# Optimization experiments

Measured on AMD Instinct MI355X. Metric: run time of the kernel, lower is better.

The kernel has to match this reference:

```python
import jax, jax.numpy as jnp
import numpy as np

HEADS = 4
HID = 128            # hidden_channels
D = HID // HEADS     # per-head dim = 32
IN = 128
OUT = 64
NEG = 0.2            # PyG HANConv default negative_slope
N_AUTHOR = 100000
N_PAPER = 200000
E = 1000000


def setup_inputs() -> dict:
    key = jax.random.key(0)
    ks = jax.random.split(key, 24)
    g = lambda i, shape, s=1.0: jax.random.normal(ks[i], shape, jnp.float32) * s
    ri = lambda i, hi: jax.random.randint(ks[i], (E,), 0, hi, dtype=jnp.int64)
    sp = float(1.0 / np.sqrt(IN))
    sh = float(1.0 / np.sqrt(HID))
    return dict(
        x_author=g(0, (N_AUTHOR, IN)),
        x_paper=g(1, (N_PAPER, IN)),
        writes_src=ri(13, N_AUTHOR), writes_dst=ri(14, N_PAPER),
        writtenby_src=ri(15, N_PAPER), writtenby_dst=ri(16, N_AUTHOR),
        cites_src=ri(17, N_PAPER), cites_dst=ri(18, N_PAPER),
        W_proj_author=g(2, (IN, HID), sp), b_proj_author=jnp.zeros((HID,), jnp.float32),
        W_proj_paper=g(3, (IN, HID), sp), b_proj_paper=jnp.zeros((HID,), jnp.float32),
        att_src_writes=g(4, (HEADS, D), sh), att_dst_writes=g(5, (HEADS, D), sh),
        att_src_writtenby=g(6, (HEADS, D), sh), att_dst_writtenby=g(7, (HEADS, D), sh),
        att_src_cites=g(8, (HEADS, D), sh), att_dst_cites=g(9, (HEADS, D), sh),
        W_k=g(10, (HID, HID), sh), b_k=jnp.zeros((HID,), jnp.float32),
        q=g(11, (HID,), sh),
        W_lin=g(12, (HID, OUT), sh), b_lin=jnp.zeros((OUT,), jnp.float32),
    )


def _edge_conv(x_src, x_dst, att_s, att_d, src, dst, n_dst):
    # x_src: [Ns,H,D], x_dst: [Nd,H,D]; gather-attend-(segment softmax)-scatter
    a_s = jnp.einsum('nhd,hd->nh', x_src, att_s)[src]   # [E,H]
    a_d = jnp.einsum('nhd,hd->nh', x_dst, att_d)[dst]   # [E,H]
    alpha = jax.nn.leaky_relu(a_s + a_d, NEG)
    m = jax.ops.segment_max(alpha, dst, num_segments=n_dst)      # [Nd,H]
    ex = jnp.exp(alpha - m[dst])
    den = jax.ops.segment_sum(ex, dst, num_segments=n_dst)
    alpha = ex / (den[dst] + 1e-16)
    msg = (x_src[src] * alpha[:, :, None]).reshape(-1, HID)      # [E,HID]
    out = jax.ops.segment_sum(msg, dst, num_segments=n_dst)      # [Nd,HID]
    return jax.nn.relu(out)


def _group(outs, q, W_k, b_k):
    # semantic-level attention over edge types (PyG HANConv `group`)
    out = jnp.stack(outs)                                         # [T,N,HID]
    score = (q * jnp.tanh(out @ W_k + b_k).mean(axis=1)).sum(-1)  # [T]
    attn = jax.nn.softmax(score)
    return jnp.einsum('t,tnc->nc', attn, out)


def reference(x_author, x_paper, writes_src, writes_dst, writtenby_src,
              writtenby_dst, cites_src, cites_dst, W_proj_author,
              b_proj_author, W_proj_paper, b_proj_paper, att_src_writes,
              att_dst_writes, att_src_writtenby, att_dst_writtenby,
              att_src_cites, att_dst_cites, W_k, b_k, q, W_lin, b_lin):
    h_a = (x_author @ W_proj_author + b_proj_author).reshape(-1, HEADS, D)
    h_p = (x_paper @ W_proj_paper + b_proj_paper).reshape(-1, HEADS, D)
    o_writes = _edge_conv(h_a, h_p, att_src_writes, att_dst_writes,
                          writes_src, writes_dst, N_PAPER)
    o_wb = _edge_conv(h_p, h_a, att_src_writtenby, att_dst_writtenby,
                      writtenby_src, writtenby_dst, N_AUTHOR)
    o_cites = _edge_conv(h_p, h_p, att_src_cites, att_dst_cites,
                         cites_src, cites_dst, N_PAPER)
    out_author = _group([o_wb], q, W_k, b_k)
    out_paper = _group([o_writes, o_cites], q, W_k, b_k)
    # final per-node-type shared Linear (HANModel.lin)
    return (out_author @ W_lin + b_lin, out_paper @ W_lin + b_lin)
```

## Files before the change

kernel.cpp:

```cpp
#include <hip/hip_runtime.h>
#include <hip/hip_bf16.h>


#define HEADS 4
#define DH 32
#define HID 128
#define IN_F 128
#define OUT_F 64
#define NEG 0.2f

typedef unsigned short u16;
typedef unsigned int u32;
typedef __attribute__((ext_vector_type(8))) short short8;
typedef __attribute__((ext_vector_type(4))) float f32x4;

__device__ __forceinline__ float us2f(u16 u){ return __uint_as_float(((u32)u) << 16); }
__device__ __forceinline__ u16 f2us(float f){
  u32 u = __float_as_uint(f);
  u += 0x7fffu + ((u >> 16) & 1u);
  return (u16)(u >> 16);
}
__device__ __forceinline__ float fin(float v){ return (fabsf(v) < 1e30f) ? v : 0.f; }
__device__ __forceinline__ u16 san16(u16 r){ return (((r >> 7) & 0xff) == 0xff) ? (u16)0 : r; }
__device__ __forceinline__ float ftanh(float x){
  float t = __expf(fminf(fmaxf(2.f * x, -30.f), 30.f));
  return __fdividef(t - 1.f, t + 1.f);
}
__device__ __forceinline__ float ldf(const void* p, size_t i, int wide){
  float v = wide ? ((const float*)p)[i] : us2f(((const u16*)p)[i]);
  return fin(v);
}
__device__ __forceinline__ u16 ld16(const void* p, size_t i, int wide){
  if (wide) return f2us(fin(((const float*)p)[i]));
  return san16(((const u16*)p)[i]);
}
__device__ __forceinline__ int ld_idx(const int* __restrict__ p, int e, int sh, int n){
  int v = p[(size_t)e << sh];
  return v < 0 ? 0 : (v >= n ? n - 1 : v);
}

__global__ void detect_float_width(const u16* __restrict__ x, int n, int* __restrict__ flag)
{
  __shared__ int cnt;
  if (threadIdx.x == 0) cnt = 0;
  __syncthreads();
  int local = 0;
  for (int i = threadIdx.x; i < n; i += blockDim.x) {
    int e = (x[i] >> 7) & 0xff;
    if (e == 0 || (e >= 100 && e <= 150)) local++;
  }
  atomicAdd(&cnt, local);
  __syncthreads();
  if (threadIdx.x == 0) *flag = (cnt < (n * 9) / 10) ? 1 : 0;
}
__global__ void detect_idx_width(const int* __restrict__ s, int n, int* __restrict__ flag)
{
  __shared__ int any;
  if (threadIdx.x == 0) any = 0;
  __syncthreads();
  for (int i = threadIdx.x; i < n; i += blockDim.x)
    if (s[2 * i + 1] != 0) atomicOr(&any, 1);
  __syncthreads();
  if (threadIdx.x == 0) *flag = any ? 0 : 1;
}

template<int NC>
__device__ __forceinline__ void stage_B1(const void* W1, int wide, u16* Bt)
{
  for (int i = threadIdx.x; i < 128 * NC; i += 256) {
    int k = i / NC, c = i - k * NC;
    u16 v = ld16(W1, (size_t)k * NC + c, wide);
    u32 boff = ((u32)c << 8) + (((u32)(k << 1)) ^ (((u32)(c & 7)) << 4));
    *(u16*)((char*)Bt + boff) = v;
  }
}

__device__ __forceinline__ short8 ldsB(const u16* Bt, int t, int lane, int kk)
{
  const int c = (t << 4) + (lane & 15);
  const u32 boff = ((u32)c << 8) +
      (((u32)(((lane >> 4) << 4) + (kk << 6))) ^ (((u32)(c & 7)) << 4));
  return *(const short8*)((const char*)Bt + boff);
}

__device__ __forceinline__ short8 ldA_x(const void* x, size_t rb, int kg, int kk, int wide)
{
  short8 v;
  const size_t base = rb + (size_t)(kg * 8 + kk * 32);
  if (wide) {
    const float* p = (const float*)x + base;
    const float4 f0 = *(const float4*)p;
    const float4 f1 = *(const float4*)(p + 4);
    v[0] = (short)f2us(fin(f0.x)); v[1] = (short)f2us(fin(f0.y));
    v[2] = (short)f2us(fin(f0.z)); v[3] = (short)f2us(fin(f0.w));
    v[4] = (short)f2us(fin(f1.x)); v[5] = (short)f2us(fin(f1.y));
    v[6] = (short)f2us(fin(f1.z)); v[7] = (short)f2us(fin(f1.w));
  } else {
    const short8 raw = *(const short8*)((const u16*)x + base);
#pragma unroll
    for (int j = 0; j < 8; ++j) v[j] = (short)san16((u16)raw[j]);
  }
  return v;
}

__device__ __forceinline__ short8 ldA_o(const u16* o, size_t rb, int kg, int kk)
{
  return *(const short8*)(o + rb + (size_t)(kg * 8 + kk * 32));
}

__global__ __launch_bounds__(256, 2) void proj_mfma(
    const void* __restrict__ x, const void* __restrict__ W,
    const void* __restrict__ b, u16* __restrict__ h, int N,
    const int* __restrict__ flag_f)
{
  const int wide = *flag_f;
  __shared__ u16 Bt[128 * 128];
  stage_B1<HID>(W, wide, Bt);
  __syncthreads();
  const int w = threadIdx.x >> 6, lane = threadIdx.x & 63;
  const int r16 = lane & 15, kg = lane >> 4;
  float bv[8];
#pragma unroll
  for (int t = 0; t < 8; ++t) bv[t] = ldf(b, (t << 4) + r16, wide);
  const int nstrips = (N + 63) >> 6;
  for (int sidx = blockIdx.x; sidx < nstrips; sidx += gridDim.x) {
    const int rowbase = (sidx << 6) + (w << 4);
    int arow = rowbase + r16;
    if (arow >= N) arow = N - 1;
    const size_t rb = (size_t)arow * IN_F;
    f32x4 acc[8];
#pragma unroll
    for (int t = 0; t < 8; ++t) acc[t] = (f32x4){0.f, 0.f, 0.f, 0.f};
#pragma unroll
    for (int kk = 0; kk < 4; ++kk) {
      const short8 a = ldA_x(x, rb, kg, kk, wide);
#pragma unroll
      for (int t = 0; t < 8; ++t)
        acc[t] = __builtin_amdgcn_mfma_f32_16x16x32_bf16(a, ldsB(Bt, t, lane, kk), acc[t], 0, 0, 0);
    }
#pragma unroll
    for (int t = 0; t < 8; ++t) {
      const int col = (t << 4) + r16;
#pragma unroll
      for (int j = 0; j < 4; ++j) {
        const int row = rowbase + (kg << 2) + j;
        if (row < N) h[(size_t)row * HID + col] = f2us(acc[t][j] + bv[t]);
      }
    }
  }
}

__global__ __launch_bounds__(256, 2) void colsum_mfma(
    const u16* __restrict__ o, int rows, const void* __restrict__ Wk,
    const void* __restrict__ bk, float* __restrict__ S,
    const int* __restrict__ flag_f)
{
  const int wide = *flag_f;
  __shared__ u16 Bt[128 * 128];
  __shared__ float sred[4][HID];
  stage_B1<HID>(Wk, wide, Bt);
  __syncthreads();
  const int w = threadIdx.x >> 6, lane = threadIdx.x & 63;
  const int r16 = lane & 15, kg = lane >> 4;
  float bkv[8];
#pragma unroll
  for (int t = 0; t < 8; ++t) bkv[t] = ldf(bk, (t << 4) + r16, wide);
  float scs[8] = {0.f, 0.f, 0.f, 0.f, 0.f, 0.f, 0.f, 0.f};
  const int nstrips = (rows + 63) >> 6;
  for (int sidx = blockIdx.x; sidx < nstrips; sidx += gridDim.x) {
    const int rowbase = (sidx << 6) + (w << 4);
    int arow = rowbase + r16;
    if (arow >= rows) arow = rows - 1;
    const size_t rb = (size_t)arow * HID;
    f32x4 acc[8];
#pragma unroll
    for (int t = 0; t < 8; ++t) acc[t] = (f32x4){0.f, 0.f, 0.f, 0.f};
#pragma unroll
    for (int kk = 0; kk < 4; ++kk) {
      const short8 a = ldA_o(o, rb, kg, kk);
#pragma unroll
      for (int t = 0; t < 8; ++t)
        acc[t] = __builtin_amdgcn_mfma_f32_16x16x32_bf16(a, ldsB(Bt, t, lane, kk), acc[t], 0, 0, 0);
    }
#pragma unroll
    for (int t = 0; t < 8; ++t) {
#pragma unroll
      for (int j = 0; j < 4; ++j) {
        const int row = rowbase + (kg << 2) + j;
        if (row < rows) scs[t] += ftanh(acc[t][j] + bkv[t]);
      }
    }
  }
#pragma unroll
  for (int t = 0; t < 8; ++t) {
    float v = scs[t];
    v += __shfl_xor(v, 16);
    v += __shfl_xor(v, 32);
    if (kg == 0) sred[w][(t << 4) + r16] = v;
  }
  __syncthreads();
  if (threadIdx.x < HID) {
    float v = sred[0][threadIdx.x] + sred[1][threadIdx.x] +
              sred[2][threadIdx.x] + sred[3][threadIdx.x];
    atomicAdd(&S[threadIdx.x], v);
  }
}

__global__ __launch_bounds__(256, 2) void linW_mfma(
    const u16* __restrict__ o, int rows, const void* __restrict__ Wlin,
    u16* __restrict__ P, const int* __restrict__ flag_f)
{
  const int wide = *flag_f;
  __shared__ u16 Bt[64 * 128];
  stage_B1<OUT_F>(Wlin, wide, Bt);
  __syncthreads();
  const int w = threadIdx.x >> 6, lane = threadIdx.x & 63;
  const int r16 = lane & 15, kg = lane >> 4;
  const int nstrips = (rows + 63) >> 6;
  for (int sidx = blockIdx.x; sidx < nstrips; sidx += gridDim.x) {
    const int rowbase = (sidx << 6) + (w << 4);
    int arow = rowbase + r16;
    if (arow >= rows) arow = rows - 1;
    const size_t rb = (size_t)arow * HID;
    f32x4 acc[4];
#pragma unroll
    for (int t = 0; t < 4; ++t) acc[t] = (f32x4){0.f, 0.f, 0.f, 0.f};
#pragma unroll
    for (int kk = 0; kk < 4; ++kk) {
      const short8 a = ldA_o(o, rb, kg, kk);
#pragma unroll
      for (int t = 0; t < 4; ++t)
        acc[t] = __builtin_amdgcn_mfma_f32_16x16x32_bf16(a, ldsB(Bt, t, lane, kk), acc[t], 0, 0, 0);
    }
#pragma unroll
    for (int t = 0; t < 4; ++t) {
      const int col = (t << 4) + r16;
#pragma unroll
      for (int j = 0; j < 4; ++j) {
        const int row = rowbase + (kg << 2) + j;
        if (row < rows) P[(size_t)row * OUT_F + col] = f2us(acc[t][j]);
      }
    }
  }
}

__global__ __launch_bounds__(256, 2) void author_mfma(
    const u16* __restrict__ o, int rows, int node0,
    const void* __restrict__ Wlin, const void* __restrict__ blin,
    void* __restrict__ out, const int* __restrict__ flag_f)
{
  const int wide = *flag_f;
  __shared__ u16 Bt[64 * 128];
  stage_B1<OUT_F>(Wlin, wide, Bt);
  __syncthreads();
  const int w = threadIdx.x >> 6, lane = threadIdx.x & 63;
  const int r16 = lane & 15, kg = lane >> 4;
  float bv[4];
#pragma unroll
  for (int t = 0; t < 4; ++t) bv[t] = ldf(blin, (t << 4) + r16, wide);
  const int nstrips = (rows + 63) >> 6;
  for (int sidx = blockIdx.x; sidx < nstrips; sidx += gridDim.x) {
    const int rowbase = (sidx << 6) + (w << 4);
    int arow = rowbase + r16;
    if (arow >= rows) arow = rows - 1;
    const size_t rb = (size_t)arow * HID;
    f32x4 acc[4];
#pragma unroll
    for (int t = 0; t < 4; ++t) acc[t] = (f32x4){0.f, 0.f, 0.f, 0.f};
#pragma unroll
    for (int kk = 0; kk < 4; ++kk) {
      const short8 a = ldA_o(o, rb, kg, kk);
#pragma unroll
      for (int t = 0; t < 4; ++t)
        acc[t] = __builtin_amdgcn_mfma_f32_16x16x32_bf16(a, ldsB(Bt, t, lane, kk), acc[t], 0, 0, 0);
    }
#pragma unroll
    for (int t = 0; t < 4; ++t) {
      const int col = (t << 4) + r16;
#pragma unroll
      for (int j = 0; j < 4; ++j) {
        const int row = rowbase + (kg << 2) + j;
        if (row < rows) {
          const float val = acc[t][j] + bv[t];
          const size_t oi = (size_t)(node0 + row) * OUT_F + col;
          if (wide) ((float*)out)[oi] = val;
          else      ((u16*)out)[oi] = f2us(val);
        }
      }
    }
  }
}

__global__ __launch_bounds__(256) void compute_a2(
    const u16* __restrict__ h, const void* __restrict__ att1,
    const void* __restrict__ att2, float* __restrict__ a1,
    float* __restrict__ a2, int N, const int* __restrict__ flag_f)
{
  const int wide = *flag_f;
  __shared__ float s1[HID], s2[HID];
  if (threadIdx.x < HID) {
    s1[threadIdx.x] = ldf(att1, threadIdx.x, wide);
    s2[threadIdx.x] = ldf(att2, threadIdx.x, wide);
  }
  __syncthreads();
  int t = blockIdx.x * 256 + threadIdx.x;
  if (t >= N * HEADS) return;
  int n = t >> 2, hh = t & 3;
  const u16* p = h + (size_t)n * HID + hh * DH;
  float acc1 = 0.f, acc2 = 0.f;
#pragma unroll
  for (int d = 0; d < DH; ++d) {
    float f = us2f(p[d]);
    acc1 += f * s1[hh * DH + d];
    acc2 += f * s2[hh * DH + d];
  }
  a1[t] = fin(acc1);
  a2[t] = fin(acc2);
}

__global__ __launch_bounds__(256) void compute_a4(
    const u16* __restrict__ h,
    const void* __restrict__ att1, const void* __restrict__ att2,
    const void* __restrict__ att3, const void* __restrict__ att4,
    float* __restrict__ a1, float* __restrict__ a2,
    float* __restrict__ a3, float* __restrict__ a4,
    int N, const int* __restrict__ flag_f)
{
  const int wide = *flag_f;
  __shared__ float s1[HID], s2[HID], s3[HID], s4[HID];
  if (threadIdx.x < HID) {
    s1[threadIdx.x] = ldf(att1, threadIdx.x, wide);
    s2[threadIdx.x] = ldf(att2, threadIdx.x, wide);
    s3[threadIdx.x] = ldf(att3, threadIdx.x, wide);
    s4[threadIdx.x] = ldf(att4, threadIdx.x, wide);
  }
  __syncthreads();
  int t = blockIdx.x * 256 + threadIdx.x;
  if (t >= N * HEADS) return;
  int n = t >> 2, hh = t & 3;
  const u16* p = h + (size_t)n * HID + hh * DH;
  float acc1 = 0.f, acc2 = 0.f, acc3 = 0.f, acc4 = 0.f;
#pragma unroll
  for (int d = 0; d < DH; ++d) {
    float f = us2f(p[d]);
    int c = hh * DH + d;
    acc1 += f * s1[c];
    acc2 += f * s2[c];
    acc3 += f * s3[c];
    acc4 += f * s4[c];
  }
  a1[t] = fin(acc1);
  a2[t] = fin(acc2);
  a3[t] = fin(acc3);
  a4[t] = fin(acc4);
}

__global__ __launch_bounds__(256) void hist3_part(
    const int* __restrict__ d0, int E0, int N0, int* __restrict__ g0,
    const int* __restrict__ d1, int E1, int N1, int* __restrict__ g1,
    const int* __restrict__ d2, int E2, int N2, int* __restrict__ g2,
    const int* __restrict__ flag_i)
{
  const int part = blockIdx.x & 7;
  const int grp  = blockIdx.x >> 3;
  const int ngrp = gridDim.x >> 3;
  const int sh = *flag_i;
  for (int e = grp * 256 + threadIdx.x; e < E0; e += ngrp * 256) {
    int d = ld_idx(d0, e, sh, N0);
    if ((d * 8) / N0 == part) atomicAdd(&g0[d], 1);
  }
  for (int e = grp * 256 + threadIdx.x; e < E1; e += ngrp * 256) {
    int d = ld_idx(d1, e, sh, N1);
    if ((d * 8) / N1 == part) atomicAdd(&g1[d], 1);
  }
  for (int e = grp * 256 + threadIdx.x; e < E2; e += ngrp * 256) {
    int d = ld_idx(d2, e, sh, N2);
    if ((d * 8) / N2 == part) atomicAdd(&g2[d], 1);
  }
}

__global__ __launch_bounds__(256) void scan1_kernel(
    const int* __restrict__ deg, int Nd, int* __restrict__ rowptr,
    int* __restrict__ blksum)
{
  __shared__ int ssum[256];
  int base = blockIdx.x * 1024;
  int t = threadIdx.x;
  int idx0 = base + t * 4;
  int v[4];
#pragma unroll
  for (int j = 0; j < 4; ++j) v[j] = (idx0 + j < Nd) ? deg[idx0 + j] : 0;
  int tsum = v[0] + v[1] + v[2] + v[3];
  ssum[t] = tsum;
  __syncthreads();
  for (int ofs = 1; ofs < 256; ofs <<= 1) {
    int x = (t >= ofs) ? ssum[t - ofs] : 0;
    __syncthreads();
    ssum[t] += x;
    __syncthreads();
  }
  if (t == 255) blksum[blockIdx.x] = ssum[255];
  int run = ssum[t] - tsum;
#pragma unroll
  for (int j = 0; j < 4; ++j) {
    if (idx0 + j < Nd) rowptr[idx0 + j] = run;
    run += v[j];
  }
}

__global__ void scan2x3_kernel(int* __restrict__ b0, int n0,
                               int* __restrict__ b1, int n1,
                               int* __restrict__ b2, int n2)
{
  if (blockIdx.x == 0) {
    if (threadIdx.x == 0) { int r = 0; for (int i = 0; i < n0; ++i) { int t = b0[i]; b0[i] = r; r += t; } }
    if (threadIdx.x == 1) { int r = 0; for (int i = 0; i < n1; ++i) { int t = b1[i]; b1[i] = r; r += t; } }
    if (threadIdx.x == 2) { int r = 0; for (int i = 0; i < n2; ++i) { int t = b2[i]; b2[i] = r; r += t; } }
  }
}

__global__ __launch_bounds__(256) void scan3_kernel(
    int* __restrict__ rowptr, int* __restrict__ cursor,
    const int* __restrict__ blksum, int Nd, int E)
{
  int i = blockIdx.x * 256 + threadIdx.x;
  if (i < Nd) {
    int v = rowptr[i] + blksum[i >> 10];
    rowptr[i] = v;
    cursor[i] = v;
  }
  if (i == 0) rowptr[Nd] = E;
}

__global__ __launch_bounds__(256) void reorder3_part(
    const int* __restrict__ s0, const int* __restrict__ d0, int E0, int Ns0, int N0,
    int* __restrict__ c0, int* __restrict__ o0,
    const int* __restrict__ s1, const int* __restrict__ d1, int E1, int Ns1, int N1,
    int* __restrict__ c1, int* __restrict__ o1,
    const int* __restrict__ s2, const int* __restrict__ d2, int E2, int Ns2, int N2,
    int* __restrict__ c2, int* __restrict__ o2,
    const int* __restrict__ flag_i)
{
  const int part = blockIdx.x & 7;
  const int grp  = blockIdx.x >> 3;
  const int ngrp = gridDim.x >> 3;
  const int sh = *flag_i;
  for (int e = grp * 256 + threadIdx.x; e < E0; e += ngrp * 256) {
    int d = ld_idx(d0, e, sh, N0);
    if ((d * 8) / N0 == part) {
      int s = ld_idx(s0, e, sh, Ns0);
      o0[atomicAdd(&c0[d], 1)] = s;
    }
  }
  for (int e = grp * 256 + threadIdx.x; e < E1; e += ngrp * 256) {
    int d = ld_idx(d1, e, sh, N1);
    if ((d * 8) / N1 == part) {
      int s = ld_idx(s1, e, sh, Ns1);
      o1[atomicAdd(&c1[d], 1)] = s;
    }
  }
  for (int e = grp * 256 + threadIdx.x; e < E2; e += ngrp * 256) {
    int d = ld_idx(d2, e, sh, N2);
    if ((d * 8) / N2 == part) {
      int s = ld_idx(s2, e, sh, Ns2);
      o2[atomicAdd(&c2[d], 1)] = s;
    }
  }
}

__global__ __launch_bounds__(256) void gather_conv(
    const int* __restrict__ rowptr, const int* __restrict__ csr_src,
    const float* __restrict__ a_s, const float* __restrict__ a_d,
    const u16* __restrict__ h_src, u16* __restrict__ o,
    int lo, int rows)
{
  int wid = (blockIdx.x * 256 + threadIdx.x) >> 6;
  if (wid >= rows) return;
  int n = lo + wid;
  int lane = threadIdx.x & 63;
  int hh = lane >> 4;
  int start = rowptr[n], end = rowptr[n + 1];
  float ad = a_d[(size_t)n * HEADS + hh];
  float m = -1e30f, den = 0.f, n0 = 0.f, n1 = 0.f;
  int e = start;
  for (; e + 4 <= end; e += 4) {
    int s0 = csr_src[e],     s1 = csr_src[e + 1];
    int s2 = csr_src[e + 2], s3 = csr_src[e + 3];
    float x0 = a_s[(size_t)s0 * HEADS + hh] + ad;
    float x1 = a_s[(size_t)s1 * HEADS + hh] + ad;
    float x2 = a_s[(size_t)s2 * HEADS + hh] + ad;
    float x3 = a_s[(size_t)s3 * HEADS + hh] + ad;
    ushort2 h0 = *(const ushort2*)(h_src + (size_t)s0 * HID + 2 * lane);
    ushort2 h1 = *(const ushort2*)(h_src + (size_t)s1 * HID + 2 * lane);
    ushort2 h2 = *(const ushort2*)(h_src + (size_t)s2 * HID + 2 * lane);
    ushort2 h3 = *(const ushort2*)(h_src + (size_t)s3 * HID + 2 * lane);
    x0 = (x0 > 0.f) ? x0 : NEG * x0;
    x1 = (x1 > 0.f) ? x1 : NEG * x1;
    x2 = (x2 > 0.f) ? x2 : NEG * x2;
    x3 = (x3 > 0.f) ? x3 : NEG * x3;
    float mloc = fmaxf(fmaxf(x0, x1), fmaxf(x2, x3));
    float mn = fmaxf(m, mloc);
    float sc = __expf(m - mn);
    float e0 = __expf(x0 - mn), e1 = __expf(x1 - mn);
    float e2 = __expf(x2 - mn), e3 = __expf(x3 - mn);
    den = den * sc + ((e0 + e1) + (e2 + e3));
    n0  = n0 * sc + (e0 * us2f(h0.x) + e1 * us2f(h1.x))
                  + (e2 * us2f(h2.x) + e3 * us2f(h3.x));
    n1  = n1 * sc + (e0 * us2f(h0.y) + e1 * us2f(h1.y))
                  + (e2 * us2f(h2.y) + e3 * us2f(h3.y));
    m = mn;
  }
  for (; e < end; ++e) {
    int s = csr_src[e];
    float x = a_s[(size_t)s * HEADS + hh] + ad;
    ushort2 hv = *(const ushort2*)(h_src + (size_t)s * HID + 2 * lane);
    x = (x > 0.f) ? x : NEG * x;
    float mn = fmaxf(m, x);
    float sc = __expf(m - mn);
    float ex = __expf(x - mn);
    den = den * sc + ex;
    n0  = n0 * sc + ex * us2f(hv.x);
    n1  = n1 * sc + ex * us2f(hv.y);
    m = mn;
  }
  float inv = 1.f / (den + 1e-16f);
  ushort2 st;
  st.x = f2us(fmaxf(n0 * inv, 0.f));
  st.y = f2us(fmaxf(n1 * inv, 0.f));
  *(ushort2*)(o + (size_t)wid * HID + 2 * lane) = st;
}

__global__ void score_softmax(const float* __restrict__ S, const void* __restrict__ q,
                              float* __restrict__ attn, float invN,
                              const int* __restrict__ flag_f)
{
  if (threadIdx.x == 0 && blockIdx.x == 0) {
    const int wide = *flag_f;
    float s0 = 0.f, s1 = 0.f;
    for (int c = 0; c < HID; ++c) {
      float qc = ldf(q, c, wide);
      s0 += qc * S[c] * invN;
      s1 += qc * S[HID + c] * invN;
    }
    float m = fmaxf(s0, s1);
    float e0 = __expf(s0 - m), e1 = __expf(s1 - m);
    attn[0] = e0 / (e0 + e1);
    attn[1] = e1 / (e0 + e1);
  }
}

__global__ __launch_bounds__(256) void combine_paper(
    const u16* __restrict__ Pw, const u16* __restrict__ Pc,
    const float* __restrict__ attn, const void* __restrict__ blin,
    void* __restrict__ out, size_t elem_off, int N,
    const int* __restrict__ flag_f)
{
  int t = blockIdx.x * 256 + threadIdx.x;
  if (t >= N * 16) return;
  const int wide = *flag_f;
  int n = t >> 4, cq = t & 15;
  const float a0 = attn[0], a1 = attn[1];
  size_t i = (size_t)n * OUT_F + cq * 4;
  ushort4 w4 = *(const ushort4*)&Pw[i];
  ushort4 c4 = *(const ushort4*)&Pc[i];
  float v[4];
  v[0] = a0 * us2f(w4.x) + a1 * us2f(c4.x) + ldf(blin, cq * 4 + 0, wide);
  v[1] = a0 * us2f(w4.y) + a1 * us2f(c4.y) + ldf(blin, cq * 4 + 1, wide);
  v[2] = a0 * us2f(w4.z) + a1 * us2f(c4.z) + ldf(blin, cq * 4 + 2, wide);
  v[3] = a0 * us2f(w4.w) + a1 * us2f(c4.w) + ldf(blin, cq * 4 + 3, wide);
  size_t oi = elem_off + i;
  if (wide) {
    float4 ov = {v[0], v[1], v[2], v[3]};
    *(float4*)&((float*)out)[oi] = ov;
  } else {
    ushort4 ov;
    ov.x = f2us(v[0]); ov.y = f2us(v[1]); ov.z = f2us(v[2]); ov.w = f2us(v[3]);
    *(ushort4*)&((u16*)out)[oi] = ov;
  }
}

extern "C" void kernel_launch(void* const* d_in, const int* in_sizes, int n_in,
                              void* d_out, int out_size, void* d_ws, size_t ws_size,
                              hipStream_t stream)
{
  const int NA = in_sizes[0] / IN_F;
  const int NP = in_sizes[1] / IN_F;
  const int E_w = in_sizes[2], E_wb = in_sizes[4], E_c = in_sizes[6];

  const void* x_a   = d_in[0];
  const void* x_p   = d_in[1];
  const int* w_src  = (const int*)d_in[2];
  const int* w_dst  = (const int*)d_in[3];
  const int* wb_src = (const int*)d_in[4];
  const int* wb_dst = (const int*)d_in[5];
  const int* c_src  = (const int*)d_in[6];
  const int* c_dst  = (const int*)d_in[7];
  const void* W_pa  = d_in[8];
  const void* b_pa  = d_in[9];
  const void* W_pp  = d_in[10];
  const void* b_pp  = d_in[11];
  const void* at_s_w  = d_in[12];
  const void* at_d_w  = d_in[13];
  const void* at_s_wb = d_in[14];
  const void* at_d_wb = d_in[15];
  const void* at_s_c  = d_in[16];
  const void* at_d_c  = d_in[17];
  const void* W_k   = d_in[18];
  const void* b_k   = d_in[19];
  const void* q     = d_in[20];
  const void* W_lin = d_in[21];
  const void* b_lin = d_in[22];

  char* ws = (char*)d_ws;
  size_t off = 0;
  auto alloc = [&](size_t bytes) -> void* {
    void* p = ws + off;
    off += (bytes + 255) & ~(size_t)255;
    return p;
  };
  int*   flag_f = (int*)alloc(4);
  int*   flag_i = (int*)alloc(4);
  float* attn   = (float*)alloc(8 * 4);
  float* S      = (float*)alloc(2 * HID * 4);
  u16*   h_a    = (u16*)alloc((size_t)NA * HID * 2);
  u16*   h_p    = (u16*)alloc((size_t)NP * HID * 2);
  float* aA_ws  = (float*)alloc((size_t)NA * HEADS * 4);
  float* aA_wbd = (float*)alloc((size_t)NA * HEADS * 4);
  float* aP_wd  = (float*)alloc((size_t)NP * HEADS * 4);
  float* aP_wbs = (float*)alloc((size_t)NP * HEADS * 4);
  float* aP_cs  = (float*)alloc((size_t)NP * HEADS * 4);
  float* aP_cd  = (float*)alloc((size_t)NP * HEADS * 4);
  u16*   Pw16   = (u16*)alloc((size_t)NP * OUT_F * 2);
  u16*   Pc16   = (u16*)alloc((size_t)NP * OUT_F * 2);
  int*   deg3   = (int*)alloc(((size_t)NP + NA + NP) * 4);
  int*   degW   = deg3;
  int*   degWB  = deg3 + NP;
  int*   degC   = deg3 + NP + NA;
  int*   rpW    = (int*)alloc(((size_t)NP + 1) * 4);
  int*   rpWB   = (int*)alloc(((size_t)NA + 1) * 4);
  int*   rpC    = (int*)alloc(((size_t)NP + 1) * 4);
  int*   curW   = (int*)alloc((size_t)NP * 4);
  int*   curWB  = (int*)alloc((size_t)NA * 4);
  int*   curC   = (int*)alloc((size_t)NP * 4);
  int*   bsW    = (int*)alloc(1024);
  int*   bsWB   = (int*)alloc(1024);
  int*   bsC    = (int*)alloc(1024);
  int*   csW    = (int*)alloc((size_t)E_w * 4);
  int*   csWB   = (int*)alloc((size_t)E_wb * 4);
  int*   csC    = (int*)alloc((size_t)E_c * 4);
  u16*   o16    = (u16*)(ws + off);
  size_t o_bytes = (ws_size > off) ? (ws_size - off) : 0;
  long long cap = (long long)(o_bytes / ((size_t)HID * 2));
  int rc = (int)(cap > NP ? NP : cap);
  rc &= ~63;
  if (rc < 64) rc = 64;

  detect_float_width<<<1, 256, 0, stream>>>((const u16*)x_a, 4096, flag_f);
  detect_idx_width<<<1, 256, 0, stream>>>(w_src, 512, flag_i);

  {
    int gA = (NA + 63) / 64; if (gA > 1024) gA = 1024;
    int gP = (NP + 63) / 64; if (gP > 1024) gP = 1024;
    proj_mfma<<<gA, 256, 0, stream>>>(x_a, W_pa, b_pa, h_a, NA, flag_f);
    proj_mfma<<<gP, 256, 0, stream>>>(x_p, W_pp, b_pp, h_p, NP, flag_f);
  }
  compute_a2<<<(NA * HEADS + 255) / 256, 256, 0, stream>>>(h_a, at_s_w, at_d_wb, aA_ws, aA_wbd, NA, flag_f);
  compute_a4<<<(NP * HEADS + 255) / 256, 256, 0, stream>>>(
      h_p, at_d_w, at_s_wb, at_s_c, at_d_c, aP_wd, aP_wbs, aP_cs, aP_cd, NP, flag_f);

  hipMemsetAsync(S, 0, 2 * HID * 4, stream);

  hipMemsetAsync(deg3, 0, ((size_t)NP + NA + NP) * 4, stream);
  {
    hist3_part<<<1024, 256, 0, stream>>>(
        w_dst, E_w, NP, degW, wb_dst, E_wb, NA, degWB, c_dst, E_c, NP, degC, flag_i);
    int nbW = (NP + 1023) / 1024, nbWB = (NA + 1023) / 1024, nbC = (NP + 1023) / 1024;
    scan1_kernel<<<nbW, 256, 0, stream>>>(degW, NP, rpW, bsW);
    scan1_kernel<<<nbWB, 256, 0, stream>>>(degWB, NA, rpWB, bsWB);
    scan1_kernel<<<nbC, 256, 0, stream>>>(degC, NP, rpC, bsC);
    scan2x3_kernel<<<1, 64, 0, stream>>>(bsW, nbW, bsWB, nbWB, bsC, nbC);
    scan3_kernel<<<(NP + 255) / 256, 256, 0, stream>>>(rpW, curW, bsW, NP, E_w);
    scan3_kernel<<<(NA + 255) / 256, 256, 0, stream>>>(rpWB, curWB, bsWB, NA, E_wb);
    scan3_kernel<<<(NP + 255) / 256, 256, 0, stream>>>(rpC, curC, bsC, NP, E_c);
    reorder3_part<<<1024, 256, 0, stream>>>(
        w_src, w_dst, E_w, NA, NP, curW, csW,
        wb_src, wb_dst, E_wb, NP, NA, curWB, csWB,
        c_src, c_dst, E_c, NP, NP, curC, csC, flag_i);
  }

  for (int lo = 0; lo < NA; lo += rc) {
    int rows = (NA - lo < rc) ? (NA - lo) : rc;
    gather_conv<<<(rows + 3) / 4, 256, 0, stream>>>(rpWB, csWB, aP_wbs, aA_wbd, h_p, o16, lo, rows);
    int g = (rows + 63) / 64; if (g > 1024) g = 1024;
    author_mfma<<<g, 256, 0, stream>>>(o16, rows, lo, W_lin, b_lin, d_out, flag_f);
  }

  for (int lo = 0; lo < NP; lo += rc) {
    int rows = (NP - lo < rc) ? (NP - lo) : rc;
    gather_conv<<<(rows + 3) / 4, 256, 0, stream>>>(rpW, csW, aA_ws, aP_wd, h_a, o16, lo, rows);
    int g = (rows + 63) / 64; if (g > 1024) g = 1024;
    colsum_mfma<<<g, 256, 0, stream>>>(o16, rows, W_k, b_k, S, flag_f);
    linW_mfma<<<g, 256, 0, stream>>>(o16, rows, W_lin, Pw16 + (size_t)lo * OUT_F, flag_f);
  }

  for (int lo = 0; lo < NP; lo += rc) {
    int rows = (NP - lo < rc) ? (NP - lo) : rc;
    gather_conv<<<(rows + 3) / 4, 256, 0, stream>>>(rpC, csC, aP_cs, aP_cd, h_p, o16, lo, rows);
    int g = (rows + 63) / 64; if (g > 1024) g = 1024;
    colsum_mfma<<<g, 256, 0, stream>>>(o16, rows, W_k, b_k, S + HID, flag_f);
    linW_mfma<<<g, 256, 0, stream>>>(o16, rows, W_lin, Pc16 + (size_t)lo * OUT_F, flag_f);
  }

  score_softmax<<<1, 64, 0, stream>>>(S, q, attn, 1.0f / (float)NP, flag_f);
  combine_paper<<<((size_t)NP * 16 + 255) / 256, 256, 0, stream>>>(Pw16, Pc16, attn, b_lin, d_out, (size_t)NA * OUT_F, NP, flag_f);
}
```

Measured before the change: 1.185 ms.

## Pre-convert edge indices to compact int32 once; raise MFMA kernel occupancy bounds

Adds a single pass that converts all six edge index arrays (possibly int64) into clamped int32 buffers. The histogram and reorder kernels then read these compact arrays directly, with no per-edge width flag and no clamping. This halves index bytes on the repeated partitioned passes (8 partitions re-read the destinations), at the cost of one extra conversion pass and more workspace, which shrinks the chunk size left for o16. It also raises launch_bounds min-blocks on the MFMA kernels, which may limit registers.

```diff
diff --git a/kernel.cpp b/kernel.cpp
--- a/kernel.cpp
+++ b/kernel.cpp
@@ -34,7 +34,7 @@
   if (wide) return f2us(fin(((const float*)p)[i]));
   return san16(((const u16*)p)[i]);
 }
-__device__ __forceinline__ int ld_idx(const int* __restrict__ p, int e, int sh, int n){
+__device__ __forceinline__ int ld_idx(const int* __restrict__ p, long long e, int sh, int n){
   int v = p[(size_t)e << sh];
   return v < 0 ? 0 : (v >= n ? n - 1 : v);
 }
@@ -62,6 +62,26 @@
     if (s[2 * i + 1] != 0) atomicOr(&any, 1);
   __syncthreads();
   if (threadIdx.x == 0) *flag = any ? 0 : 1;
+}
+
+__global__ __launch_bounds__(256) void cvt_idx6(
+    const int* __restrict__ p0, int n0, int c0, int* __restrict__ q0,
+    const int* __restrict__ p1, int n1, int c1, int* __restrict__ q1,
+    const int* __restrict__ p2, int n2, int c2, int* __restrict__ q2,
+    const int* __restrict__ p3, int n3, int c3, int* __restrict__ q3,
+    const int* __restrict__ p4, int n4, int c4, int* __restrict__ q4,
+    const int* __restrict__ p5, int n5, int c5, int* __restrict__ q5,
+    const int* __restrict__ flag_i)
+{
+  const int sh = *flag_i;
+  const int t = blockIdx.x * 256 + threadIdx.x;
+  const int stride = gridDim.x * 256;
+  for (int e = t; e < n0; e += stride) q0[e] = ld_idx(p0, e, sh, c0);
+  for (int e = t; e < n1; e += stride) q1[e] = ld_idx(p1, e, sh, c1);
+  for (int e = t; e < n2; e += stride) q2[e] = ld_idx(p2, e, sh, c2);
+  for (int e = t; e < n3; e += stride) q3[e] = ld_idx(p3, e, sh, c3);
+  for (int e = t; e < n4; e += stride) q4[e] = ld_idx(p4, e, sh, c4);
+  for (int e = t; e < n5; e += stride) q5[e] = ld_idx(p5, e, sh, c5);
 }
 
 template<int NC>
@@ -108,7 +128,7 @@
   return *(const short8*)(o + rb + (size_t)(kg * 8 + kk * 32));
 }
 
-__global__ __launch_bounds__(256, 2) void proj_mfma(
+__global__ __launch_bounds__(256, 4) void proj_mfma(
     const void* __restrict__ x, const void* __restrict__ W,
     const void* __restrict__ b, u16* __restrict__ h, int N,
     const int* __restrict__ flag_f)
@@ -150,7 +170,7 @@
   }
 }
 
-__global__ __launch_bounds__(256, 2) void colsum_mfma(
+__global__ __launch_bounds__(256, 3) void colsum_mfma(
     const u16* __restrict__ o, int rows, const void* __restrict__ Wk,
     const void* __restrict__ bk, float* __restrict__ S,
     const int* __restrict__ flag_f)
@@ -206,7 +226,7 @@
   }
 }
 
-__global__ __launch_bounds__(256, 2) void linW_mfma(
+__global__ __launch_bounds__(256, 4) void linW_mfma(
     const u16* __restrict__ o, int rows, const void* __restrict__ Wlin,
     u16* __restrict__ P, const int* __restrict__ flag_f)
 {
@@ -244,7 +264,7 @@
   }
 }
 
-__global__ __launch_bounds__(256, 2) void author_mfma(
+__global__ __launch_bounds__(256, 4) void author_mfma(
     const u16* __restrict__ o, int rows, int node0,
     const void* __restrict__ Wlin, const void* __restrict__ blin,
     void* __restrict__ out, const int* __restrict__ flag_f)
@@ -358,23 +378,21 @@
 __global__ __launch_bounds__(256) void hist3_part(
     const int* __restrict__ d0, int E0, int N0, int* __restrict__ g0,
     const int* __restrict__ d1, int E1, int N1, int* __restrict__ g1,
-    const int* __restrict__ d2, int E2, int N2, int* __restrict__ g2,
-    const int* __restrict__ flag_i)
+    const int* __restrict__ d2, int E2, int N2, int* __restrict__ g2)
 {
   const int part = blockIdx.x & 7;
   const int grp  = blockIdx.x >> 3;
   const int ngrp = gridDim.x >> 3;
-  const int sh = *flag_i;
   for (int e = grp * 256 + threadIdx.x; e < E0; e += ngrp * 256) {
-    int d = ld_idx(d0, e, sh, N0);
+    int d = d0[e];
     if ((d * 8) / N0 == part) atomicAdd(&g0[d], 1);
   }
   for (int e = grp * 256 + threadIdx.x; e < E1; e += ngrp * 256) {
-    int d = ld_idx(d1, e, sh, N1);
+    int d = d1[e];
     if ((d * 8) / N1 == part) atomicAdd(&g1[d], 1);
   }
   for (int e = grp * 256 + threadIdx.x; e < E2; e += ngrp * 256) {
-    int d = ld_idx(d2, e, sh, N2);
+    int d = d2[e];
     if ((d * 8) / N2 == part) atomicAdd(&g2[d], 1);
   }
 }
@@ -433,38 +451,27 @@
 }
 
 __global__ __launch_bounds__(256) void reorder3_part(
-    const int* __restrict__ s0, const int* __restrict__ d0, int E0, int Ns0, int N0,
+    const int* __restrict__ s0, const int* __restrict__ d0, int E0, int N0,
     int* __restrict__ c0, int* __restrict__ o0,
-    const int* __restrict__ s1, const int* __restrict__ d1, int E1, int Ns1, int N1,
+    const int* __restrict__ s1, const int* __restrict__ d1, int E1, int N1,
     int* __restrict__ c1, int* __restrict__ o1,
-    const int* __restrict__ s2, const int* __restrict__ d2, int E2, int Ns2, int N2,
-    int* __restrict__ c2, int* __restrict__ o2,
-    const int* __restrict__ flag_i)
+    const int* __restrict__ s2, const int* __restrict__ d2, int E2, int N2,
+    int* __restrict__ c2, int* __restrict__ o2)
 {
   const int part = blockIdx.x & 7;
   const int grp  = blockIdx.x >> 3;
   const int ngrp = gridDim.x >> 3;
-  const int sh = *flag_i;
   for (int e = grp * 256 + threadIdx.x; e < E0; e += ngrp * 256) {
-    int d = ld_idx(d0, e, sh, N0);
-    if ((d * 8) / N0 == part) {
-      int s = ld_idx(s0, e, sh, Ns0);
-      o0[atomicAdd(&c0[d], 1)] = s;
-    }
+    int d = d0[e];
+    if ((d * 8) / N0 == part) o0[atomicAdd(&c0[d], 1)] = s0[e];
   }
   for (int e = grp * 256 + threadIdx.x; e < E1; e += ngrp * 256) {
-    int d = ld_idx(d1, e, sh, N1);
-    if ((d * 8) / N1 == part) {
-      int s = ld_idx(s1, e, sh, Ns1);
-      o1[atomicAdd(&c1[d], 1)] = s;
-    }
+    int d = d1[e];
+    if ((d * 8) / N1 == part) o1[atomicAdd(&c1[d], 1)] = s1[e];
   }
   for (int e = grp * 256 + threadIdx.x; e < E2; e += ngrp * 256) {
-    int d = ld_idx(d2, e, sh, N2);
-    if ((d * 8) / N2 == part) {
-      int s = ld_idx(s2, e, sh, Ns2);
-      o2[atomicAdd(&c2[d], 1)] = s;
-    }
+    int d = d2[e];
+    if ((d * 8) / N2 == part) o2[atomicAdd(&c2[d], 1)] = s2[e];
   }
 }
 
@@ -632,6 +639,12 @@
   float* aP_cd  = (float*)alloc((size_t)NP * HEADS * 4);
   u16*   Pw16   = (u16*)alloc((size_t)NP * OUT_F * 2);
   u16*   Pc16   = (u16*)alloc((size_t)NP * OUT_F * 2);
+  int*   wS32   = (int*)alloc((size_t)E_w * 4);
+  int*   wD32   = (int*)alloc((size_t)E_w * 4);
+  int*   wbS32  = (int*)alloc((size_t)E_wb * 4);
+  int*   wbD32  = (int*)alloc((size_t)E_wb * 4);
+  int*   cS32   = (int*)alloc((size_t)E_c * 4);
+  int*   cD32   = (int*)alloc((size_t)E_c * 4);
   int*   deg3   = (int*)alloc(((size_t)NP + NA + NP) * 4);
   int*   degW   = deg3;
   int*   degWB  = deg3 + NP;
@@ -658,6 +671,11 @@
   detect_float_width<<<1, 256, 0, stream>>>((const u16*)x_a, 4096, flag_f);
   detect_idx_width<<<1, 256, 0, stream>>>(w_src, 512, flag_i);
 
+  cvt_idx6<<<2048, 256, 0, stream>>>(
+      w_src, E_w, NA, wS32,   w_dst, E_w, NP, wD32,
+      wb_src, E_wb, NP, wbS32, wb_dst, E_wb, NA, wbD32,
+      c_src, E_c, NP, cS32,   c_dst, E_c, NP, cD32, flag_i);
+
   {
     int gA = (NA + 63) / 64; if (gA > 1024) gA = 1024;
     int gP = (NP + 63) / 64; if (gP > 1024) gP = 1024;
@@ -673,7 +691,7 @@
   hipMemsetAsync(deg3, 0, ((size_t)NP + NA + NP) * 4, stream);
   {
     hist3_part<<<1024, 256, 0, stream>>>(
-        w_dst, E_w, NP, degW, wb_dst, E_wb, NA, degWB, c_dst, E_c, NP, degC, flag_i);
+        wD32, E_w, NP, degW, wbD32, E_wb, NA, degWB, cD32, E_c, NP, degC);
     int nbW = (NP + 1023) / 1024, nbWB = (NA + 1023) / 1024, nbC = (NP + 1023) / 1024;
     scan1_kernel<<<nbW, 256, 0, stream>>>(degW, NP, rpW, bsW);
     scan1_kernel<<<nbWB, 256, 0, stream>>>(degWB, NA, rpWB, bsWB);
@@ -683,9 +701,9 @@
     scan3_kernel<<<(NA + 255) / 256, 256, 0, stream>>>(rpWB, curWB, bsWB, NA, E_wb);
     scan3_kernel<<<(NP + 255) / 256, 256, 0, stream>>>(rpC, curC, bsC, NP, E_c);
     reorder3_part<<<1024, 256, 0, stream>>>(
-        w_src, w_dst, E_w, NA, NP, curW, csW,
-        wb_src, wb_dst, E_wb, NP, NA, curWB, csWB,
-        c_src, c_dst, E_c, NP, NP, curC, csC, flag_i);
+        wS32, wD32, E_w, NP, curW, csW,
+        wbS32, wbD32, E_wb, NA, curWB, csWB,
+        cS32, cD32, E_c, NP, curC, csC);
   }
 
   for (int lo = 0; lo < NA; lo += rc) {
```

After: 1.288 ms. 8.7% more time.
